# Kernel optimization log

Hardware: AMD Instinct MI355X
Metric: run time of the kernel (lower is better)

Reference implementation:

```python
import jax, jax.numpy as jnp
import numpy as np

N_NODES = 10000
N_EDGES = 320000
F = 256   # node_feat_dim
H = 256   # node_hidden_dim
ED = 64   # edge_embed_dim


def _message_passing(x, edge_index, edge_features, W, b):
    # x: [N, H], edge_index: [2, E], edge_features: [E, ED]
    src, dst = edge_index[0], edge_index[1]
    m = jnp.concatenate([x[src], x[dst], edge_features], axis=-1)  # [E, 2H+ED]
    m = jax.nn.gelu(m @ W + b)                                     # [E, H]
    agg = jax.ops.segment_sum(m, dst, num_segments=N_NODES)        # [N, H]
    return x + agg


def setup_inputs() -> dict:
    key = jax.random.key(0)
    ks = jax.random.split(key, 12)
    s = 0.02
    return {
        "x": jax.random.normal(ks[0], (N_NODES, F), dtype=jnp.float32),
        "edge_index": jax.random.randint(ks[1], (2, N_EDGES), 0, N_NODES, dtype=jnp.int64),
        "edge_features": jax.random.normal(ks[2], (N_EDGES, ED), dtype=jnp.float32),
        "W_ff1": jax.random.normal(ks[3], (F, H), dtype=jnp.float32) * s,
        "b_ff1": jnp.zeros((H,), dtype=jnp.float32),
        "W_mp1": jax.random.normal(ks[4], (2 * H + ED, H), dtype=jnp.float32) * s,
        "b_mp1": jnp.zeros((H,), dtype=jnp.float32),
        "W_mp2": jax.random.normal(ks[5], (2 * H + ED, H), dtype=jnp.float32) * s,
        "b_mp2": jnp.zeros((H,), dtype=jnp.float32),
        "W_ff2": jax.random.normal(ks[6], (H, F), dtype=jnp.float32) * s,
        "b_ff2": jnp.zeros((F,), dtype=jnp.float32),
    }


def reference(x, edge_index, edge_features, W_ff1, b_ff1, W_mp1, b_mp1, W_mp2, b_mp2, W_ff2, b_ff2):
    residual = x
    h = jax.nn.gelu(x @ W_ff1 + b_ff1)                       # FFN1 + GELU
    h = _message_passing(h, edge_index, edge_features, W_mp1, b_mp1)
    h = _message_passing(h, edge_index, edge_features, W_mp2, b_mp2)
    return residual + (h @ W_ff2 + b_ff2)                    # FFN2 + residual
```

## Files before the change

### kernel.cpp

```cpp
#include <hip/hip_runtime.h>


typedef __attribute__((ext_vector_type(8))) short short8;
typedef __attribute__((ext_vector_type(4))) float f32x4;

#define HD __device__ __forceinline__

HD unsigned short f2bf(float f) {
    unsigned int u = __float_as_uint(f);
    return (unsigned short)((u + 0x7fffu + ((u >> 16) & 1u)) >> 16);
}
HD float lo16(unsigned int u) { return __uint_as_float(u << 16); }
HD float hi16(unsigned int u) { return __uint_as_float(u & 0xffff0000u); }
HD float bf2f(unsigned short u) { return __uint_as_float(((unsigned int)u) << 16); }

HD float gelu_f(float x) {
    float u = x * (-1.5957691216057308f - 0.07135481627f * (x * x));
    return x * __builtin_amdgcn_rcpf(1.f + __expf(u));
}

__global__ void repack_all(const float* __restrict__ Wff1,
                           const float* __restrict__ Wmp1,
                           const float* __restrict__ Wmp2,
                           const float* __restrict__ Wff2,
                           unsigned short* __restrict__ Bp) {
    const int begs[9] = {0, 65536, 131072, 196608, 212992, 278528, 344064,
                         360448, 425984};
    const int srcid[8] = {0, 1, 1, 1, 2, 2, 2, 3};
    const int rowoff[8] = {0, 0, 256, 512, 0, 256, 512, 0};
    int i = blockIdx.x * 256 + threadIdx.x;
    if (i >= 425984) return;
    int s = 0;
#pragma unroll
    for (int k = 1; k < 8; ++k)
        if (i >= begs[k]) s = k;
    const float* Ws[4] = {Wff1, Wmp1, Wmp2, Wff2};
    const float* B = Ws[srcid[s]];
    int local = i - begs[s];
    int k = local >> 8, n = local & 255;
    int kb = k >> 5, kr = k & 31;
    int quad = kr >> 3, j = kr & 7;
    int lane = quad * 16 + (n & 15);
    int nt = n >> 4;
    Bp[begs[s] + ((((kb * 16 + nt) * 64) + lane) << 3) + j] =
        f2bf(B[(size_t)(rowoff[s] + k) * 256 + n]);
}

__global__ __launch_bounds__(256) void gemm_kernel(
    const void* __restrict__ Av, int a_is_f32, int M, int K,
    const unsigned short* __restrict__ Bp,
    const float* __restrict__ bias, const float* __restrict__ resid,
    unsigned short* __restrict__ Cb, float* __restrict__ Cf, int do_gelu) {
    int lane = threadIdx.x & 63;
    int w = threadIdx.x >> 6;
    int row0 = blockIdx.x * 64 + w * 16;
    int n0 = blockIdx.y * 64;
    int m15 = lane & 15, quad = lane >> 4;

    int arow = row0 + m15;
    if (arow > M - 1) arow = M - 1;

    f32x4 acc[4] = {{0,0,0,0},{0,0,0,0},{0,0,0,0},{0,0,0,0}};
    const float* Af = (const float*)Av + (size_t)arow * K + quad * 8;
    const unsigned short* Ab = (const unsigned short*)Av + (size_t)arow * K + quad * 8;

    for (int kt = 0; kt < K; kt += 32) {
        short8 a;
        if (a_is_f32) {
            f32x4 lo = *(const f32x4*)(Af + kt);
            f32x4 hi = *(const f32x4*)(Af + kt + 4);
#pragma unroll
            for (int j = 0; j < 4; ++j) {
                a[j] = (short)f2bf(lo[j]);
                a[j + 4] = (short)f2bf(hi[j]);
            }
        } else {
            a = *(const short8*)(Ab + kt);
        }
        const unsigned short* bbase =
            Bp + ((((size_t)(kt >> 5) * 16 + (n0 >> 4)) * 64 + lane) << 3);
#pragma unroll
        for (int nt = 0; nt < 4; ++nt) {
            short8 b = *(const short8*)(bbase + nt * 64 * 8);
            acc[nt] = __builtin_amdgcn_mfma_f32_16x16x32_bf16(a, b, acc[nt], 0, 0, 0);
        }
    }

#pragma unroll
    for (int nt = 0; nt < 4; ++nt) {
        int col = n0 + nt * 16 + m15;
        float bv = bias ? bias[col] : 0.f;
#pragma unroll
        for (int r = 0; r < 4; ++r) {
            int row = row0 + quad * 4 + r;
            if (row < M) {
                float v = acc[nt][r] + bv;
                if (do_gelu) v = gelu_f(v);
                size_t idx = (size_t)row * 256 + col;
                if (resid) v += resid[idx];
                if (Cb) Cb[idx] = f2bf(v);
                if (Cf) Cf[idx] = v;
            }
        }
    }
}

__global__ __launch_bounds__(256) void pq_kernel(
    const unsigned short* __restrict__ A, int M,
    const unsigned short* __restrict__ BpA, const unsigned short* __restrict__ BpB,
    const float* __restrict__ qbias,
    unsigned short* __restrict__ Pb, unsigned short* __restrict__ Qb) {
    int lane = threadIdx.x & 63;
    int w = threadIdx.x >> 6;
    int row0 = blockIdx.x * 64 + w * 16;
    int isQ = blockIdx.y >> 2;
    int n0 = (blockIdx.y & 3) * 64;
    const unsigned short* Bp = isQ ? BpB : BpA;
    unsigned short* out = isQ ? Qb : Pb;
    int m15 = lane & 15, quad = lane >> 4;

    int arow = row0 + m15;
    if (arow > M - 1) arow = M - 1;
    const unsigned short* Ab = A + (size_t)arow * 256 + quad * 8;

    f32x4 acc[4] = {{0,0,0,0},{0,0,0,0},{0,0,0,0},{0,0,0,0}};
    for (int kt = 0; kt < 256; kt += 32) {
        short8 a = *(const short8*)(Ab + kt);
        const unsigned short* bbase =
            Bp + ((((size_t)(kt >> 5) * 16 + (n0 >> 4)) * 64 + lane) << 3);
#pragma unroll
        for (int nt = 0; nt < 4; ++nt) {
            short8 b = *(const short8*)(bbase + nt * 64 * 8);
            acc[nt] = __builtin_amdgcn_mfma_f32_16x16x32_bf16(a, b, acc[nt], 0, 0, 0);
        }
    }

#pragma unroll
    for (int nt = 0; nt < 4; ++nt) {
        int col = n0 + nt * 16 + m15;
        float bv = isQ ? qbias[col] : 0.f;
#pragma unroll
        for (int r = 0; r < 4; ++r) {
            int row = row0 + quad * 4 + r;
            if (row < M) out[(size_t)row * 256 + col] = f2bf(acc[nt][r] + bv);
        }
    }
}

__global__ void zero_i32(int* __restrict__ p, int n) {
    int i = blockIdx.x * 256 + threadIdx.x;
    if (i < n) p[i] = 0;
}
__global__ void hist_kernel(const int* __restrict__ dst, int* __restrict__ cnt, int E) {
    int e = blockIdx.x * 256 + threadIdx.x;
    if (e < E) atomicAdd(&cnt[dst[e]], 1);
}
__global__ __launch_bounds__(1024) void scan_kernel(const int* __restrict__ cnt,
                                                    int* __restrict__ cursor, int N) {
    __shared__ int part[1024];
    int tid = threadIdx.x;
    int per = (N + 1023) / 1024;
    int lo = tid * per;
    int s = 0;
    for (int j = 0; j < per; ++j) {
        int idx = lo + j;
        if (idx < N) s += cnt[idx];
    }
    part[tid] = s;
    __syncthreads();
    for (int off = 1; off < 1024; off <<= 1) {
        int t = (tid >= off) ? part[tid - off] : 0;
        __syncthreads();
        part[tid] += t;
        __syncthreads();
    }
    int run = (tid > 0) ? part[tid - 1] : 0;
    for (int j = 0; j < per; ++j) {
        int idx = lo + j;
        if (idx < N) {
            cursor[idx] = run;
            run += cnt[idx];
        }
    }
}
__global__ void scatter_kernel(const int* __restrict__ src, const int* __restrict__ dst,
                               int* __restrict__ cursor, int* __restrict__ perm,
                               int* __restrict__ srcs, int* __restrict__ dsts, int E) {
    int e = blockIdx.x * 256 + threadIdx.x;
    if (e < E) {
        int d = dst[e];
        int pos = atomicAdd(&cursor[d], 1);
        perm[pos] = e;
        srcs[pos] = src[e];
        dsts[pos] = d;
    }
}

__global__ __launch_bounds__(256, 4) void fused_kernel(
    const float* __restrict__ ef, const int* __restrict__ perm,
    const int* __restrict__ srcs, const int* __restrict__ dsts,
    const unsigned short* __restrict__ BpC,
    const unsigned short* __restrict__ Pb, const unsigned short* __restrict__ Qb,
    const int* __restrict__ cursor, const int* __restrict__ cnt,
    float* __restrict__ Hacc, int E) {
    __shared__ unsigned short tiles[64 * 256];
    float* Fr = (float*)tiles;
    float* Lr = Fr + 4 * 256;
    int* Cd = (int*)(Lr + 4 * 256);

    int lane = threadIdx.x & 63;
    int w = threadIdx.x >> 6;
    int e_lo = blockIdx.x * 64;
    int n_e = E - e_lo;
    if (n_e > 64) n_e = 64;
    int e_hi = e_lo + n_e;
    int base = w * 16;
    int m15 = lane & 15, quad = lane >> 4;
    int c0 = lane << 2;

    int myi = base + (lane & 15);
    int mye = e_lo + myi;
    if (mye > E - 1) mye = E - 1;
    int vsw = srcs[mye];
    int vdw = dsts[mye];

    int cur_d = -2;
    uint2 qu = {0u, 0u};
    if (base < n_e) {
        cur_d = __builtin_amdgcn_readlane(vdw, 0);
        qu = *(const uint2*)(Qb + (((size_t)cur_d) << 8) + c0);
    }
    int fd_first = cur_d;

    {
        int ar = e_lo + base + m15;
        if (ar > E - 1) ar = E - 1;
        int g = perm[ar];
        const float* A = ef + (size_t)g * 64 + quad * 8;

        f32x4 acc[16];
#pragma unroll
        for (int i = 0; i < 16; ++i) acc[i] = {0.f, 0.f, 0.f, 0.f};

#pragma unroll
        for (int kb = 0; kb < 2; ++kb) {
            f32x4 lo = *(const f32x4*)(A + kb * 32);
            f32x4 hi = *(const f32x4*)(A + kb * 32 + 4);
            short8 a;
#pragma unroll
            for (int j = 0; j < 4; ++j) {
                a[j] = (short)f2bf(lo[j]);
                a[j + 4] = (short)f2bf(hi[j]);
            }
            const unsigned short* bb = BpC + (((size_t)kb * 16 * 64 + lane) << 3);
#pragma unroll
            for (int nt = 0; nt < 16; ++nt) {
                short8 b = *(const short8*)(bb + (size_t)nt * 64 * 8);
                acc[nt] = __builtin_amdgcn_mfma_f32_16x16x32_bf16(a, b, acc[nt], 0, 0, 0);
            }
        }

#pragma unroll
        for (int nt = 0; nt < 16; ++nt) {
            int colp = ((nt ^ quad) << 4) + m15;
#pragma unroll
            for (int r = 0; r < 4; ++r) {
                int row = base + quad * 4 + r;
                tiles[row * 256 + colp] = f2bf(acc[nt][r]);
            }
        }
    }

    float s0 = 0.f, s1 = 0.f, s2 = 0.f, s3 = 0.f;
    float F0 = 0.f, F1 = 0.f, F2 = 0.f, F3 = 0.f;
    int lastd = -2;
    int emitted = 0;

    if (n_e == 64) {
        uint2 pu[16], ru[16];
#pragma unroll
        for (int j = 0; j < 16; ++j) {
            int s = __builtin_amdgcn_readlane(vsw, j);
            pu[j] = *(const uint2*)(Pb + (((size_t)s) << 8) + c0);
            int k = base + j;
            int off = (((lane >> 2) ^ ((j >> 2) & 3)) << 4) + ((lane & 3) << 2);
            ru[j] = *(const uint2*)(tiles + k * 256 + off);
        }
#pragma unroll
        for (int j = 0; j < 16; ++j) {
            if (j > 0) {
                int d = __builtin_amdgcn_readlane(vdw, j);
                if (d != cur_d) {
                    if (!emitted) {
                        F0 = s0; F1 = s1; F2 = s2; F3 = s3;
                        emitted = 1;
                    } else {
                        float* hp = Hacc + (((size_t)cur_d) << 8) + c0;
                        hp[0] += s0; hp[1] += s1; hp[2] += s2; hp[3] += s3;
                    }
                    s0 = s1 = s2 = s3 = 0.f;
                    cur_d = d;
                    qu = *(const uint2*)(Qb + (((size_t)d) << 8) + c0);
                }
            }
            float q0 = lo16(qu.x), q1 = hi16(qu.x);
            float q2 = lo16(qu.y), q3 = hi16(qu.y);
            s0 += gelu_f(lo16(pu[j].x) + q0 + lo16(ru[j].x));
            s1 += gelu_f(hi16(pu[j].x) + q1 + hi16(ru[j].x));
            s2 += gelu_f(lo16(pu[j].y) + q2 + lo16(ru[j].y));
            s3 += gelu_f(hi16(pu[j].y) + q3 + hi16(ru[j].y));
        }
        if (!emitted) {
            F0 = s0; F1 = s1; F2 = s2; F3 = s3;
            lastd = -2;
        } else {
            lastd = cur_d;
        }
    } else {
        int lim = n_e - base;
        if (lim < 0) lim = 0;
        if (lim > 16) lim = 16;
        if (lim == 0) { fd_first = -2; lastd = -2; }
        for (int j = 0; j < lim; ++j) {
            if (j > 0) {
                int d = __builtin_amdgcn_readlane(vdw, j);
                if (d != cur_d) {
                    if (!emitted) {
                        F0 = s0; F1 = s1; F2 = s2; F3 = s3;
                        emitted = 1;
                    } else {
                        float* hp = Hacc + (((size_t)cur_d) << 8) + c0;
                        hp[0] += s0; hp[1] += s1; hp[2] += s2; hp[3] += s3;
                    }
                    s0 = s1 = s2 = s3 = 0.f;
                    cur_d = d;
                    qu = *(const uint2*)(Qb + (((size_t)d) << 8) + c0);
                }
            }
            int s = __builtin_amdgcn_readlane(vsw, j);
            uint2 pv = *(const uint2*)(Pb + (((size_t)s) << 8) + c0);
            int k = base + j;
            int off = (((lane >> 2) ^ ((k >> 2) & 3)) << 4) + ((lane & 3) << 2);
            uint2 rv = *(const uint2*)(tiles + k * 256 + off);
            s0 += gelu_f(lo16(pv.x) + lo16(qu.x) + lo16(rv.x));
            s1 += gelu_f(hi16(pv.x) + hi16(qu.x) + hi16(rv.x));
            s2 += gelu_f(lo16(pv.y) + lo16(qu.y) + lo16(rv.y));
            s3 += gelu_f(hi16(pv.y) + hi16(qu.y) + hi16(rv.y));
        }
        if (lim > 0) {
            if (!emitted) {
                F0 = s0; F1 = s1; F2 = s2; F3 = s3;
                lastd = -2;
            } else {
                lastd = cur_d;
            }
        }
    }

    __syncthreads();

    Fr[w * 256 + c0 + 0] = F0;
    Fr[w * 256 + c0 + 1] = F1;
    Fr[w * 256 + c0 + 2] = F2;
    Fr[w * 256 + c0 + 3] = F3;
    Lr[w * 256 + c0 + 0] = s0;
    Lr[w * 256 + c0 + 1] = s1;
    Lr[w * 256 + c0 + 2] = s2;
    Lr[w * 256 + c0 + 3] = s3;
    if (lane == 0) {
        Cd[w] = fd_first;
        Cd[4 + w] = lastd;
    }
    __syncthreads();

    {
        int ch = threadIdx.x;
        float rv = 0.f;
        int rd = -1;
#pragma unroll
        for (int i = 0; i < 8; ++i) {
            int wi = i >> 1;
            int d = (i & 1) ? Cd[4 + wi] : Cd[wi];
            if (d < 0) continue;
            float v = (i & 1) ? Lr[wi * 256 + ch] : Fr[wi * 256 + ch];
            if (d == rd) {
                rv += v;
            } else {
                if (rd >= 0) {
                    int end = cursor[rd], beg = end - cnt[rd];
                    size_t hidx = (((size_t)rd) << 8) + ch;
                    if (beg >= e_lo && end <= e_hi)
                        Hacc[hidx] += rv;
                    else
                        atomicAdd(&Hacc[hidx], rv);
                }
                rd = d;
                rv = v;
            }
        }
        if (rd >= 0) {
            int end = cursor[rd], beg = end - cnt[rd];
            size_t hidx = (((size_t)rd) << 8) + ch;
            if (beg >= e_lo && end <= e_hi)
                Hacc[hidx] += rv;
            else
                atomicAdd(&Hacc[hidx], rv);
        }
    }
}

__global__ void finalize_h(const float* __restrict__ Hacc,
                           unsigned short* __restrict__ h_bf, int n4) {
    int i = blockIdx.x * 256 + threadIdx.x;
    if (i < n4) {
        float4 v = ((const float4*)Hacc)[i];
        uint2 o;
        o.x = (unsigned int)f2bf(v.x) | ((unsigned int)f2bf(v.y) << 16);
        o.y = (unsigned int)f2bf(v.z) | ((unsigned int)f2bf(v.w) << 16);
        ((uint2*)h_bf)[i] = o;
    }
}

extern "C" void kernel_launch(void* const* d_in, const int* in_sizes, int n_in,
                              void* d_out, int out_size, void* d_ws, size_t ws_size,
                              hipStream_t stream) {
    const float* x     = (const float*)d_in[0];
    const int*   ei    = (const int*)d_in[1];
    const float* ef    = (const float*)d_in[2];
    const float* W_ff1 = (const float*)d_in[3];
    const float* b_ff1 = (const float*)d_in[4];
    const float* W_mp1 = (const float*)d_in[5];
    const float* b_mp1 = (const float*)d_in[6];
    const float* W_mp2 = (const float*)d_in[7];
    const float* b_mp2 = (const float*)d_in[8];
    const float* W_ff2 = (const float*)d_in[9];
    const float* b_ff2 = (const float*)d_in[10];

    const int N = in_sizes[0] / 256;
    const int E = in_sizes[1] / 2;
    const int* src = ei;
    const int* dst = ei + E;

    char* p = (char*)d_ws;
    unsigned short* h_bf = (unsigned short*)p;  p += ((size_t)N * 256 * 2 + 255) & ~255ull;
    unsigned short* Pbuf = (unsigned short*)p;  p += ((size_t)N * 256 * 2 + 255) & ~255ull;
    unsigned short* Qbuf = (unsigned short*)p;  p += ((size_t)N * 256 * 2 + 255) & ~255ull;
    float* Hacc = (float*)p;                    p += ((size_t)N * 256 * 4 + 255) & ~255ull;
    unsigned short* Bp = (unsigned short*)p;    p += (425984ull * 2 + 255) & ~255ull;
    int* cnt    = (int*)p;                      p += ((size_t)N * 4 + 255) & ~255ull;
    int* cursor = (int*)p;                      p += ((size_t)N * 4 + 255) & ~255ull;
    int* perm   = (int*)p;                      p += ((size_t)E * 4 + 255) & ~255ull;
    int* srcs   = (int*)p;                      p += ((size_t)E * 4 + 255) & ~255ull;
    int* dsts   = (int*)p;                      p += ((size_t)E * 4 + 255) & ~255ull;

    unsigned short* Bp_ff1 = Bp + 0;
    unsigned short* Bp_a1  = Bp + 65536;
    unsigned short* Bp_b1  = Bp + 131072;
    unsigned short* Bp_c1  = Bp + 196608;
    unsigned short* Bp_a2  = Bp + 212992;
    unsigned short* Bp_b2  = Bp + 278528;
    unsigned short* Bp_c2  = Bp + 344064;
    unsigned short* Bp_ff2 = Bp + 360448;

    repack_all<<<1664, 256, 0, stream>>>(W_ff1, W_mp1, W_mp2, W_ff2, Bp);

    zero_i32<<<(N + 255) / 256, 256, 0, stream>>>(cnt, N);
    hist_kernel<<<(E + 255) / 256, 256, 0, stream>>>(dst, cnt, E);
    scan_kernel<<<1, 1024, 0, stream>>>(cnt, cursor, N);
    scatter_kernel<<<(E + 255) / 256, 256, 0, stream>>>(src, dst, cursor, perm, srcs,
                                                        dsts, E);

    dim3 gN((N + 63) / 64, 4);
    dim3 gPQ((N + 63) / 64, 8);
    int n_tiles = (E + 63) / 64;

    gemm_kernel<<<gN, 256, 0, stream>>>(x, 1, N, 256, Bp_ff1, b_ff1, nullptr,
                                        h_bf, Hacc, 1);

    const unsigned short* Bp_a[2] = {Bp_a1, Bp_a2};
    const unsigned short* Bp_b[2] = {Bp_b1, Bp_b2};
    const unsigned short* Bp_c[2] = {Bp_c1, Bp_c2};
    const float* bmp[2] = {b_mp1, b_mp2};

    for (int l = 0; l < 2; ++l) {
        pq_kernel<<<gPQ, 256, 0, stream>>>(h_bf, N, Bp_a[l], Bp_b[l], bmp[l],
                                           Pbuf, Qbuf);
        fused_kernel<<<n_tiles, 256, 0, stream>>>(
            ef, perm, srcs, dsts, Bp_c[l], Pbuf, Qbuf, cursor, cnt, Hacc, E);
        if (l == 0)
            finalize_h<<<(N * 64 + 255) / 256, 256, 0, stream>>>(Hacc, h_bf, N * 64);
    }

    gemm_kernel<<<gN, 256, 0, stream>>>(Hacc, 1, N, 256, Bp_ff2, b_ff2, x,
                                        nullptr, (float*)d_out, 0);
}
```

Before: 412.7 us.

## Fuse FFN1 with first P/Q projection and convert hidden state inside PQ kernel

Combines the FFN1 GEMM and the layer-1 P/Q projections into one kernel that keeps the GELU output tile in shared memory as bf16 and reuses it as the A operand. For layer 2, a new pq2 kernel reads the fp32 accumulator directly and converts it to bf16 in registers, which removes the finalize_h pass and the h_bf buffer. Each block is now a single 64-thread wave covering 16 rows and all 256 columns for both P and Q. This cuts launches and intermediate traffic, but lowers per-block parallelism and raises register pressure (16 accumulator tiles plus 8 A fragments).

Result: slower. 512.2 us (+24.1%).

```diff
diff --git a/kernel.cpp b/kernel.cpp
--- a/kernel.cpp
+++ b/kernel.cpp
@@ -105,44 +105,142 @@
     }
 }
 
-__global__ __launch_bounds__(256) void pq_kernel(
-    const unsigned short* __restrict__ A, int M,
+__global__ __launch_bounds__(64) void ffn1pq_kernel(
+    const float* __restrict__ x, const unsigned short* __restrict__ BpF,
+    const float* __restrict__ bff1,
+    const unsigned short* __restrict__ BpA, const unsigned short* __restrict__ BpB,
+    const float* __restrict__ qbias, float* __restrict__ Hacc,
+    unsigned short* __restrict__ Pb, unsigned short* __restrict__ Qb, int M) {
+    __shared__ unsigned short hl[16 * 264];
+    int lane = threadIdx.x;
+    int m15 = lane & 15, quad = lane >> 4;
+    int row0 = blockIdx.x * 16;
+
+    int arow = row0 + m15;
+    if (arow > M - 1) arow = M - 1;
+    const float* Af = x + (size_t)arow * 256 + quad * 8;
+
+    f32x4 acc[16];
+#pragma unroll
+    for (int nt = 0; nt < 16; ++nt) acc[nt] = {0.f, 0.f, 0.f, 0.f};
+#pragma unroll
+    for (int kt = 0; kt < 256; kt += 32) {
+        f32x4 lo = *(const f32x4*)(Af + kt);
+        f32x4 hi = *(const f32x4*)(Af + kt + 4);
+        short8 a;
+#pragma unroll
+        for (int j = 0; j < 4; ++j) {
+            a[j] = (short)f2bf(lo[j]);
+            a[j + 4] = (short)f2bf(hi[j]);
+        }
+        const unsigned short* bb = BpF + ((((size_t)(kt >> 5) * 16) * 64 + lane) << 3);
+#pragma unroll
+        for (int nt = 0; nt < 16; ++nt) {
+            short8 b = *(const short8*)(bb + (size_t)nt * 64 * 8);
+            acc[nt] = __builtin_amdgcn_mfma_f32_16x16x32_bf16(a, b, acc[nt], 0, 0, 0);
+        }
+    }
+#pragma unroll
+    for (int nt = 0; nt < 16; ++nt) {
+        int col = nt * 16 + m15;
+        float bv = bff1[col];
+#pragma unroll
+        for (int r = 0; r < 4; ++r) {
+            int lrow = quad * 4 + r;
+            float v = gelu_f(acc[nt][r] + bv);
+            if (row0 + lrow < M) Hacc[(size_t)(row0 + lrow) * 256 + col] = v;
+            hl[lrow * 264 + col] = f2bf(v);
+        }
+    }
+
+    short8 afrag[8];
+#pragma unroll
+    for (int kt8 = 0; kt8 < 8; ++kt8)
+        afrag[kt8] = *(const short8*)(hl + m15 * 264 + quad * 8 + kt8 * 32);
+
+#pragma unroll
+    for (int pass = 0; pass < 2; ++pass) {
+        const unsigned short* Bw = pass ? BpB : BpA;
+        unsigned short* out = pass ? Qb : Pb;
+#pragma unroll
+        for (int nt = 0; nt < 16; ++nt) acc[nt] = {0.f, 0.f, 0.f, 0.f};
+#pragma unroll
+        for (int kt8 = 0; kt8 < 8; ++kt8) {
+            const unsigned short* bb =
+                Bw + ((((size_t)(kt8 >> 1) * 16) * 64 + lane) << 3) + (kt8 & 1) * 0;
+            bb = Bw + ((((size_t)kt8 * 16) * 64 + lane) << 3);
+#pragma unroll
+            for (int nt = 0; nt < 16; ++nt) {
+                short8 b = *(const short8*)(bb + (size_t)nt * 64 * 8);
+                acc[nt] = __builtin_amdgcn_mfma_f32_16x16x32_bf16(afrag[kt8], b,
+                                                                  acc[nt], 0, 0, 0);
+            }
+        }
+#pragma unroll
+        for (int nt = 0; nt < 16; ++nt) {
+            int col = nt * 16 + m15;
+            float bv = pass ? qbias[col] : 0.f;
+#pragma unroll
+            for (int r = 0; r < 4; ++r) {
+                int row = row0 + quad * 4 + r;
+                if (row < M) out[(size_t)row * 256 + col] = f2bf(acc[nt][r] + bv);
+            }
+        }
+    }
+}
+
+__global__ __launch_bounds__(64) void pq2_kernel(
+    const float* __restrict__ Hin,
     const unsigned short* __restrict__ BpA, const unsigned short* __restrict__ BpB,
     const float* __restrict__ qbias,
-    unsigned short* __restrict__ Pb, unsigned short* __restrict__ Qb) {
-    int lane = threadIdx.x & 63;
-    int w = threadIdx.x >> 6;
-    int row0 = blockIdx.x * 64 + w * 16;
-    int isQ = blockIdx.y >> 2;
-    int n0 = (blockIdx.y & 3) * 64;
-    const unsigned short* Bp = isQ ? BpB : BpA;
-    unsigned short* out = isQ ? Qb : Pb;
+    unsigned short* __restrict__ Pb, unsigned short* __restrict__ Qb, int M) {
+    int lane = threadIdx.x;
     int m15 = lane & 15, quad = lane >> 4;
-
+    int row0 = blockIdx.x * 16;
     int arow = row0 + m15;
     if (arow > M - 1) arow = M - 1;
-    const unsigned short* Ab = A + (size_t)arow * 256 + quad * 8;
-
-    f32x4 acc[4] = {{0,0,0,0},{0,0,0,0},{0,0,0,0},{0,0,0,0}};
-    for (int kt = 0; kt < 256; kt += 32) {
-        short8 a = *(const short8*)(Ab + kt);
-        const unsigned short* bbase =
-            Bp + ((((size_t)(kt >> 5) * 16 + (n0 >> 4)) * 64 + lane) << 3);
-#pragma unroll
-        for (int nt = 0; nt < 4; ++nt) {
-            short8 b = *(const short8*)(bbase + nt * 64 * 8);
-            acc[nt] = __builtin_amdgcn_mfma_f32_16x16x32_bf16(a, b, acc[nt], 0, 0, 0);
-        }
-    }
-
-#pragma unroll
-    for (int nt = 0; nt < 4; ++nt) {
-        int col = n0 + nt * 16 + m15;
-        float bv = isQ ? qbias[col] : 0.f;
-#pragma unroll
-        for (int r = 0; r < 4; ++r) {
-            int row = row0 + quad * 4 + r;
-            if (row < M) out[(size_t)row * 256 + col] = f2bf(acc[nt][r] + bv);
+    const float* Af = Hin + (size_t)arow * 256 + quad * 8;
+
+    short8 afrag[8];
+#pragma unroll
+    for (int kt8 = 0; kt8 < 8; ++kt8) {
+        f32x4 lo = *(const f32x4*)(Af + kt8 * 32);
+        f32x4 hi = *(const f32x4*)(Af + kt8 * 32 + 4);
+        short8 a;
+#pragma unroll
+        for (int j = 0; j < 4; ++j) {
+            a[j] = (short)f2bf(lo[j]);
+            a[j + 4] = (short)f2bf(hi[j]);
+        }
+        afrag[kt8] = a;
+    }
+
+    f32x4 acc[16];
+#pragma unroll
+    for (int pass = 0; pass < 2; ++pass) {
+        const unsigned short* Bw = pass ? BpB : BpA;
+        unsigned short* out = pass ? Qb : Pb;
+#pragma unroll
+        for (int nt = 0; nt < 16; ++nt) acc[nt] = {0.f, 0.f, 0.f, 0.f};
+#pragma unroll
+        for (int kt8 = 0; kt8 < 8; ++kt8) {
+            const unsigned short* bb = Bw + ((((size_t)kt8 * 16) * 64 + lane) << 3);
+#pragma unroll
+            for (int nt = 0; nt < 16; ++nt) {
+                short8 b = *(const short8*)(bb + (size_t)nt * 64 * 8);
+                acc[nt] = __builtin_amdgcn_mfma_f32_16x16x32_bf16(afrag[kt8], b,
+                                                                  acc[nt], 0, 0, 0);
+            }
+        }
+#pragma unroll
+        for (int nt = 0; nt < 16; ++nt) {
+            int col = nt * 16 + m15;
+            float bv = pass ? qbias[col] : 0.f;
+#pragma unroll
+            for (int r = 0; r < 4; ++r) {
+                int row = row0 + quad * 4 + r;
+                if (row < M) out[(size_t)row * 256 + col] = f2bf(acc[nt][r] + bv);
+            }
         }
     }
 }
@@ -409,18 +507,6 @@
     }
 }
 
-__global__ void finalize_h(const float* __restrict__ Hacc,
-                           unsigned short* __restrict__ h_bf, int n4) {
-    int i = blockIdx.x * 256 + threadIdx.x;
-    if (i < n4) {
-        float4 v = ((const float4*)Hacc)[i];
-        uint2 o;
-        o.x = (unsigned int)f2bf(v.x) | ((unsigned int)f2bf(v.y) << 16);
-        o.y = (unsigned int)f2bf(v.z) | ((unsigned int)f2bf(v.w) << 16);
-        ((uint2*)h_bf)[i] = o;
-    }
-}
-
 extern "C" void kernel_launch(void* const* d_in, const int* in_sizes, int n_in,
                               void* d_out, int out_size, void* d_ws, size_t ws_size,
                               hipStream_t stream) {
@@ -442,7 +528,6 @@
     const int* dst = ei + E;
 
     char* p = (char*)d_ws;
-    unsigned short* h_bf = (unsigned short*)p;  p += ((size_t)N * 256 * 2 + 255) & ~255ull;
     unsigned short* Pbuf = (unsigned short*)p;  p += ((size_t)N * 256 * 2 + 255) & ~255ull;
     unsigned short* Qbuf = (unsigned short*)p;  p += ((size_t)N * 256 * 2 + 255) & ~255ull;
     float* Hacc = (float*)p;                    p += ((size_t)N * 256 * 4 + 255) & ~255ull;
@@ -470,27 +555,19 @@
     scatter_kernel<<<(E + 255) / 256, 256, 0, stream>>>(src, dst, cursor, perm, srcs,
                                                         dsts, E);
 
+    int n_tiles = (E + 63) / 64;
+    int n_rb = (N + 15) / 16;
+
+    ffn1pq_kernel<<<n_rb, 64, 0, stream>>>(x, Bp_ff1, b_ff1, Bp_a1, Bp_b1,
+                                           b_mp1, Hacc, Pbuf, Qbuf, N);
+    fused_kernel<<<n_tiles, 256, 0, stream>>>(
+        ef, perm, srcs, dsts, Bp_c1, Pbuf, Qbuf, cursor, cnt, Hacc, E);
+
+    pq2_kernel<<<n_rb, 64, 0, stream>>>(Hacc, Bp_a2, Bp_b2, b_mp2, Pbuf, Qbuf, N);
+    fused_kernel<<<n_tiles, 256, 0, stream>>>(
+        ef, perm, srcs, dsts, Bp_c2, Pbuf, Qbuf, cursor, cnt, Hacc, E);
+
     dim3 gN((N + 63) / 64, 4);
-    dim3 gPQ((N + 63) / 64, 8);
-    int n_tiles = (E + 63) / 64;
-
-    gemm_kernel<<<gN, 256, 0, stream>>>(x, 1, N, 256, Bp_ff1, b_ff1, nullptr,
-                                        h_bf, Hacc, 1);
-
-    const unsigned short* Bp_a[2] = {Bp_a1, Bp_a2};
-    const unsigned short* Bp_b[2] = {Bp_b1, Bp_b2};
-    const unsigned short* Bp_c[2] = {Bp_c1, Bp_c2};
-    const float* bmp[2] = {b_mp1, b_mp2};
-
-    for (int l = 0; l < 2; ++l) {
-        pq_kernel<<<gPQ, 256, 0, stream>>>(h_bf, N, Bp_a[l], Bp_b[l], bmp[l],
-                                           Pbuf, Qbuf);
-        fused_kernel<<<n_tiles, 256, 0, stream>>>(
-            ef, perm, srcs, dsts, Bp_c[l], Pbuf, Qbuf, cursor, cnt, Hacc, E);
-        if (l == 0)
-            finalize_h<<<(N * 64 + 255) / 256, 256, 0, stream>>>(Hacc, h_bf, N * 64);
-    }
-
     gemm_kernel<<<gN, 256, 0, stream>>>(Hacc, 1, N, 256, Bp_ff2, b_ff2, x,
                                         nullptr, (float*)d_out, 0);
 }
```
